# Optimization experiments

Hardware: AMD Instinct MI355X
Metric: run time of the kernel (lower is better)

Reference implementation:

```python
import jax, jax.numpy as jnp
import numpy as np

BN_EPS = 1e-5
NORM_EPS = 1e-12  # F.normalize eps
NUM_HEADS = 8
QUERY_DIM = 256
TOP_K = 16


def _l2norm(x):
    n = jnp.linalg.norm(x, axis=-1, keepdims=True)
    return x / jnp.maximum(n, NORM_EPS)


def setup_inputs() -> dict:
    key = jax.random.key(0)
    ks = jax.random.split(key, 8)
    B, S, D, O, N = 2, 512, 1024, 1024, 16384
    return {
        "hidden_states": jax.random.normal(ks[0], (B, S, D), jnp.float32),
        "Wq": jax.random.normal(ks[1], (D, NUM_HEADS * QUERY_DIM), jnp.float32) * 0.02,
        "bq": jnp.zeros((NUM_HEADS * QUERY_DIM,), jnp.float32),
        "bn_gamma": jnp.ones((QUERY_DIM,), jnp.float32),
        "bn_beta": jnp.zeros((QUERY_DIM,), jnp.float32),
        "sub_keys0": jax.random.normal(ks[2], (128, 128), jnp.float32) * 0.02,
        "sub_keys1": jax.random.normal(ks[3], (128, 128), jnp.float32) * 0.02,
        "expert_down": jax.random.normal(ks[4], (N, D), jnp.float32) * 0.02,
        "expert_up": jax.random.normal(ks[5], (N, O), jnp.float32) * 0.02,
    }


def reference(hidden_states, Wq, bq, bn_gamma, bn_beta, sub_keys0, sub_keys1, expert_down, expert_up):
    B, S, D = hidden_states.shape
    H, QD, K = NUM_HEADS, QUERY_DIM, TOP_K

    # query projection -> [B,S,H,QD]
    q = (hidden_states @ Wq + bq).reshape(B, S, H, QD)

    # BatchNorm1d over flattened (B*S*H, QD), training-mode batch stats (biased var)
    qf = q.reshape(-1, QD)
    mean = qf.mean(axis=0)
    var = qf.var(axis=0)
    qf = (qf - mean) * jax.lax.rsqrt(var + BN_EPS) * bn_gamma + bn_beta
    q = qf.reshape(B, S, H, QD)

    # split query into two halves, L2-normalize queries and keys, sub-scores
    half = QD // 2
    s0 = jnp.einsum('bshd,nd->bshn', _l2norm(q[..., :half]), _l2norm(sub_keys0))  # [B,S,H,128]
    s1 = jnp.einsum('bshd,nd->bshn', _l2norm(q[..., half:]), _l2norm(sub_keys1))  # [B,S,H,128]

    # cartesian-product scores: flat expert idx = i*128 + j (matches meshgrid 'ij')
    total = (s0[..., :, None] + s1[..., None, :]).reshape(B, S, H, -1)  # [B,S,H,16384]

    top_scores, top_idx = jax.lax.top_k(total, K)  # [B,S,H,K]
    w = jax.nn.softmax(top_scores, axis=-1)

    dw = expert_down[top_idx]  # [B,S,H,K,D]  (expert_hidden_size = 1)
    uw = expert_up[top_idx]    # [B,S,H,K,O]

    ei = jnp.einsum('bshkd,bsd->bshk', dw, hidden_states)  # per-expert scalar hidden
    eo = jax.nn.gelu(ei, approximate=False)                # F.gelu default = erf
    out = jnp.einsum('bshko,bshk,bshk->bso', uw, eo, w)    # weighted sum over K and H
    return out
```

## Files before the change

kernel.cpp:

```cpp
#include <hip/hip_runtime.h>
#include <math.h>

typedef unsigned long long u64;
typedef unsigned int u32;
typedef unsigned short ushort_t;
typedef _Float16 half8 __attribute__((ext_vector_type(8)));
typedef float f32x4 __attribute__((ext_vector_type(4)));

#define TOKENS 1024
#define DDIM   1024
#define NHEAD  8
#define QD     256
#define HQD    2048
#define NROWS  8192
#define NKEY   128
#define TOPK   16

#define QSCALE 256.0f
#define QINVS  (1.0f / 65536.0f)

__device__ __forceinline__ ushort_t f2bf(float f) {
    u32 u = __float_as_uint(f);
    u32 r = (u + 0x7FFFu + ((u >> 16) & 1u)) >> 16;
    return (ushort_t)r;
}
__device__ __forceinline__ float bf_lo(u32 w) { return __uint_as_float(w << 16); }
__device__ __forceinline__ float bf_hi(u32 w) { return __uint_as_float(w & 0xFFFF0000u); }

__device__ __forceinline__ void hsplit(float x, ushort_t& h, ushort_t& l) {
    _Float16 hh = (_Float16)x;
    float r = x - (float)hh;
    _Float16 ll = (_Float16)r;
    union { _Float16 f; ushort_t u; } c1, c2;
    c1.f = hh; c2.f = ll;
    h = c1.u; l = c2.u;
}

__device__ __forceinline__ u32 ordf(float v) {
    u32 u = __float_as_uint(v);
    return (u & 0x80000000u) ? ~u : (u | 0x80000000u);
}
__device__ __forceinline__ u64 mkkey2(float v, u32 idx) {
    return ((u64)ordf(v) << 32) | (u64)(0xFFFFFFFFu - idx);
}

template<int NTHR, int ITERS>
__device__ __forceinline__ void cvt_chunk(int gcb, int tid,
                                          const float* __restrict__ down,
                                          const float* __restrict__ up,
                                          ushort_t* __restrict__ downb,
                                          ushort_t* __restrict__ upb) {
    const float* src = (gcb < 1024) ? down : up;
    ushort_t* dst = (gcb < 1024) ? downb : upb;
    const size_t base4 = (size_t)(gcb & 1023) * 4096;
    const float4* s4 = (const float4*)src;
    ushort4* d4 = (ushort4*)dst;
#pragma unroll 4
    for (int it = 0; it < ITERS; it++) {
        size_t i = base4 + (size_t)it * NTHR + tid;
        float4 v = s4[i];
        ushort4 o;
        o.x = f2bf(v.x); o.y = f2bf(v.y); o.z = f2bf(v.z); o.w = f2bf(v.w);
        d4[i] = o;
    }
}

__global__ __launch_bounds__(256) void k_prep1(
    const float* __restrict__ A, const float* __restrict__ W,
    ushort_t* __restrict__ Ab, ushort_t* __restrict__ Wt,
    const float* __restrict__ sk0, const float* __restrict__ sk1,
    float* __restrict__ k0n, float* __restrict__ k1n)
{
    __shared__ __align__(16) char praw[18464];
    const int bid = blockIdx.x;
    const int tid = threadIdx.x;

    if (bid < 128) {
#pragma unroll
        for (int i = 0; i < 8; i++) {
            const int row = bid * 8 + i;
            float4 v = *(const float4*)(A + (size_t)row * 1024 + tid * 4);
            ushort4 h, l;
            hsplit(v.x * QSCALE, h.x, l.x);
            hsplit(v.y * QSCALE, h.y, l.y);
            hsplit(v.z * QSCALE, h.z, l.z);
            hsplit(v.w * QSCALE, h.w, l.w);
            *(ushort4*)(Ab + (size_t)row * 2048 + tid * 4) = h;
            *(ushort4*)(Ab + (size_t)row * 2048 + 1024 + tid * 4) = l;
        }
    } else if (bid < 640) {
        const int cb = bid - 128;
        const int k0 = (cb >> 5) * 64;
        const int n0 = (cb & 31) * 64;
        ushort_t* Lh = (ushort_t*)praw;
        ushort_t* Ll = (ushort_t*)praw + 4608;
        const int nn = (tid & 15) * 4;
        const int kk = tid >> 4;
#pragma unroll
        for (int p = 0; p < 4; p++) {
            const int k = kk + 16 * p;
            float4 v = *(const float4*)(W + (size_t)(k0 + k) * HQD + n0 + nn);
            float xs[4] = {v.x * QSCALE, v.y * QSCALE, v.z * QSCALE, v.w * QSCALE};
#pragma unroll
            for (int j = 0; j < 4; j++) {
                ushort_t h, l;
                hsplit(xs[j], h, l);
                Lh[(nn + j) * 72 + k] = h;
                Ll[(nn + j) * 72 + k] = l;
            }
        }
        __syncthreads();
#pragma unroll
        for (int e = 0; e < 2; e++) {
            const int idx = tid + 256 * e;
            const int n = idx >> 3, ks = idx & 7;
            uint4 hv = *(const uint4*)(Lh + n * 72 + ks * 8);
            uint4 lv = *(const uint4*)(Ll + n * 72 + ks * 8);
            *(uint4*)(Wt + (size_t)(n0 + n) * 2048 + k0 + ks * 8) = hv;
            *(uint4*)(Wt + (size_t)(n0 + n) * 2048 + 1024 + k0 + ks * 8) = lv;
        }
    } else {
        float* fs = (float*)praw;
        const int b2 = bid - 640;
        const int sub = tid >> 7;
        const int col = tid & 127;
        const int gr = b2 * 2 + sub;
        const float* src = (gr < 128) ? sk0 : sk1;
        float* dst = (gr < 128) ? k0n : k1n;
        const int row = gr & 127;
        float v = src[row * 128 + col];
        float sq = v * v;
        for (int off = 32; off; off >>= 1) sq += __shfl_down(sq, off);
        if ((tid & 63) == 0) fs[tid >> 6] = sq;
        __syncthreads();
        if ((tid & 127) == 0) {
            float n = sqrtf(fs[tid >> 6] + fs[(tid >> 6) + 1]);
            fs[8 + sub] = 1.0f / fmaxf(n, 1e-12f);
        }
        __syncthreads();
        dst[row * 128 + col] = v * fs[8 + sub];
    }
}

__global__ __launch_bounds__(256) void k_fused2(
    const ushort_t* __restrict__ Ab, const ushort_t* __restrict__ Wt,
    float* __restrict__ qp,
    const float* __restrict__ down, const float* __restrict__ up,
    ushort_t* __restrict__ downb, ushort_t* __restrict__ upb)
{
    __shared__ __align__(16) char lds[2][16384];
    const int tid = threadIdx.x;
    const int bid = blockIdx.x;

    if (bid >= 512) {
        cvt_chunk<256, 16>(bid - 512, tid, down, up, downb, upb);
        return;
    }

    const int m0 = (bid >> 5) * 64;
    const int n0 = (bid & 31) * 64;

    const int srow = tid >> 2;
    const int scol = (tid & 3) * 16;
    const int swz = (srow & 7) << 4;

    const int lane = tid & 63;
    const int w = tid >> 6;
    const int wmb = (w >> 1) * 32;
    const int wnb = (w & 1) * 32;
    const int fr = lane & 15;
    const int kg = lane >> 4;
    const int rswz = (fr & 7) << 4;

    f32x4 acc[2][2];
#pragma unroll
    for (int i = 0; i < 2; i++)
#pragma unroll
        for (int j = 0; j < 2; j++)
            acc[i][j] = (f32x4){0.f, 0.f, 0.f, 0.f};

    uint4 ar0, ar1, br0, br1;

    auto LOADR = [&](int gs) {
        const int term = gs >> 4;
        const int aoff = (term == 1) ? 1024 : 0;
        const int woff = (term == 2) ? 1024 : 0;
        const int kb = (gs & 15) * 64;
        const ushort_t* ap = Ab + (size_t)(m0 + srow) * 2048 + aoff + kb + scol;
        const ushort_t* wp = Wt + (size_t)(n0 + srow) * 2048 + woff + kb + scol;
        ar0 = *(const uint4*)(ap);
        ar1 = *(const uint4*)(ap + 8);
        br0 = *(const uint4*)(wp);
        br1 = *(const uint4*)(wp + 8);
    };
    auto WLDS = [&](int buf) {
        char* As = lds[buf];
        char* Bs = lds[buf] + 8192;
        const int b0 = (srow * 128 + scol * 2) ^ swz;
        const int b1 = (srow * 128 + scol * 2 + 16) ^ swz;
        *(uint4*)(As + b0) = ar0;
        *(uint4*)(As + b1) = ar1;
        *(uint4*)(Bs + b0) = br0;
        *(uint4*)(Bs + b1) = br1;
    };

    LOADR(0);
    WLDS(0);

    for (int s = 0; s < 48; s++) {
        __syncthreads();
        if (s < 47) LOADR(s + 1);
        const char* As = lds[s & 1];
        const char* Bs = lds[s & 1] + 8192;
#pragma unroll
        for (int kh = 0; kh < 2; kh++) {
            half8 a[2], b[2];
#pragma unroll
            for (int f = 0; f < 2; f++) {
                const int rowA = wmb + f * 16 + fr;
                a[f] = *(const half8*)(As + ((rowA * 128 + kh * 64 + kg * 16) ^ rswz));
                const int rowB = wnb + f * 16 + fr;
                b[f] = *(const half8*)(Bs + ((rowB * 128 + kh * 64 + kg * 16) ^ rswz));
            }
#pragma unroll
            for (int fm = 0; fm < 2; fm++)
#pragma unroll
                for (int fn = 0; fn < 2; fn++)
                    acc[fm][fn] = __builtin_amdgcn_mfma_f32_16x16x32_f16(
                        a[fm], b[fn], acc[fm][fn], 0, 0, 0);
        }
        if (s < 47) WLDS((s + 1) & 1);
    }

#pragma unroll
    for (int fm = 0; fm < 2; fm++) {
        const int rbase = m0 + wmb + fm * 16 + kg * 4;
#pragma unroll
        for (int fn = 0; fn < 2; fn++) {
            const int c = n0 + wnb + fn * 16 + fr;
#pragma unroll
            for (int j = 0; j < 4; j++)
                qp[(size_t)(rbase + j) * HQD + c] = acc[fm][fn][j];
        }
    }
}

__global__ __launch_bounds__(256) void k_bnstat1(const float* __restrict__ qp,
                                                 const float* __restrict__ bq,
                                                 float* __restrict__ psum,
                                                 float* __restrict__ psq,
                                                 float qsc,
                                                 const float* __restrict__ down,
                                                 const float* __restrict__ up,
                                                 ushort_t* __restrict__ downb,
                                                 ushort_t* __restrict__ upb)
{
    const int b = blockIdx.x;
    const int j = threadIdx.x;
    if (b >= 512) {
        cvt_chunk<256, 16>(512 + (b - 512), j, down, up, downb, upb);
        return;
    }
    float s = 0.f, sq = 0.f;
#pragma unroll 4
    for (int rr = 0; rr < 16; rr++) {
        const int r = b * 16 + rr;
        const size_t g = (size_t)r * 256 + j;
        float v = qp[g] * qsc + bq[(r & 7) * 256 + j];
        s += v; sq += v * v;
    }
    psum[b * 256 + j] = s;
    psq[b * 256 + j]  = sq;
}

__global__ __launch_bounds__(256) void k_bnstat2(const float* __restrict__ psum,
                                                 const float* __restrict__ psq,
                                                 const float* __restrict__ gamma,
                                                 float* __restrict__ meanOut,
                                                 float* __restrict__ scaleOut)
{
    __shared__ float ls[8][64];
    const int col = blockIdx.x * 32 + (threadIdx.x & 31);
    const int seg = threadIdx.x >> 5;
    float s = 0.f, sq = 0.f;
    for (int b = seg; b < 512; b += 8) {
        s += psum[b * 256 + col];
        sq += psq[b * 256 + col];
    }
    ls[seg][(threadIdx.x & 31)] = s;
    ls[seg][32 + (threadIdx.x & 31)] = sq;
    __syncthreads();
    if (threadIdx.x < 32) {
        float ts = 0.f, tq = 0.f;
#pragma unroll
        for (int g = 0; g < 8; g++) {
            ts += ls[g][threadIdx.x];
            tq += ls[g][32 + threadIdx.x];
        }
        float mean = ts * (1.0f / 8192.0f);
        float var = tq * (1.0f / 8192.0f) - mean * mean;
        meanOut[col] = mean;
        scaleOut[col] = gamma[col] / sqrtf(var + 1e-5f);
    }
}

__global__ __launch_bounds__(256) void k_scores(const float* __restrict__ qp,
                                                const float* __restrict__ bq,
                                                const float* __restrict__ mean,
                                                const float* __restrict__ scale,
                                                const float* __restrict__ beta,
                                                const float* __restrict__ kn0,
                                                const float* __restrict__ kn1,
                                                float* __restrict__ sOut0,
                                                float* __restrict__ sOut1,
                                                float qsc,
                                                const float* __restrict__ down,
                                                const float* __restrict__ up,
                                                ushort_t* __restrict__ downb,
                                                ushort_t* __restrict__ upb)
{
    __shared__ float Qs[128 * 68];
    __shared__ float Ks[64 * 132];
    __shared__ float rp[4][64];
    __shared__ float invn[64];
    const int bid = blockIdx.x;
    const int tid = threadIdx.x;
    if (bid >= 256) {
        cvt_chunk<256, 16>(768 + (bid - 256), tid, down, up, downb, upb);
        return;
    }
    const int half = bid >> 7;
    const int row0 = (bid & 127) * 64;

    {
        const int d4 = (tid & 31) * 4;
        const int rbase = tid >> 5;
        const int j4 = half * 128 + d4;
        float4 m4 = *(const float4*)(mean + j4);
        float4 sc4 = *(const float4*)(scale + j4);
        float4 be4 = *(const float4*)(beta + j4);
        float4 bi4 = *(const float4*)(bq + rbase * 256 + j4);
#pragma unroll
        for (int p = 0; p < 8; p++) {
            const int rr = rbase + p * 8;
            const int row = row0 + rr;
            const size_t g = (size_t)(row >> 3) * 2048 + (size_t)rbase * 256 + j4;
            float4 a = *(const float4*)(qp + g);
            float x0 = (a.x * qsc + bi4.x - m4.x) * sc4.x + be4.x;
            float x1 = (a.y * qsc + bi4.y - m4.y) * sc4.y + be4.y;
            float x2 = (a.z * qsc + bi4.z - m4.z) * sc4.z + be4.z;
            float x3 = (a.w * qsc + bi4.w - m4.w) * sc4.w + be4.w;
            Qs[(d4 + 0) * 68 + rr] = x0;
            Qs[(d4 + 1) * 68 + rr] = x1;
            Qs[(d4 + 2) * 68 + rr] = x2;
            Qs[(d4 + 3) * 68 + rr] = x3;
        }
    }
    __syncthreads();
    {
        const int r = tid & 63, qd = tid >> 6;
        float s = 0.f;
#pragma unroll 8
        for (int d = qd * 32; d < qd * 32 + 32; d++) {
            float v = Qs[d * 68 + r];
            s += v * v;
        }
        rp[qd][r] = s;
    }
    __syncthreads();
    if (tid < 64) {
        float s = rp[0][tid] + rp[1][tid] + rp[2][tid] + rp[3][tid];
        invn[tid] = 1.0f / fmaxf(sqrtf(s), 1e-12f);
    }

    const float* kn = half ? kn1 : kn0;
    float* sOut = half ? sOut1 : sOut0;
    const int ty = tid >> 5;
    const int tx = tid & 31;
    float acc[8][4] = {};

    for (int c = 0; c < 2; c++) {
        __syncthreads();
        {
            int dd4 = (tid & 15) * 4;
            int n = tid >> 4;
#pragma unroll
            for (int p = 0; p < 8; p++) {
                int nn = n + p * 16;
                float4 v = *(const float4*)(kn + nn * 128 + c * 64 + dd4);
                Ks[(dd4 + 0) * 132 + nn] = v.x; Ks[(dd4 + 1) * 132 + nn] = v.y;
                Ks[(dd4 + 2) * 132 + nn] = v.z; Ks[(dd4 + 3) * 132 + nn] = v.w;
            }
        }
        __syncthreads();
#pragma unroll
        for (int d = 0; d < 64; d++) {
            float a[8], b[4];
            *(float4*)(a)     = *(const float4*)&Qs[(c * 64 + d) * 68 + ty * 8];
            *(float4*)(a + 4) = *(const float4*)&Qs[(c * 64 + d) * 68 + ty * 8 + 4];
            *(float4*)(b)     = *(const float4*)&Ks[d * 132 + tx * 4];
#pragma unroll
            for (int i = 0; i < 8; i++)
#pragma unroll
                for (int j = 0; j < 4; j++)
                    acc[i][j] = fmaf(a[i], b[j], acc[i][j]);
        }
    }
#pragma unroll
    for (int i = 0; i < 8; i++) {
        const float iv = invn[ty * 8 + i];
        float4 r;
        r.x = acc[i][0] * iv; r.y = acc[i][1] * iv;
        r.z = acc[i][2] * iv; r.w = acc[i][3] * iv;
        *(float4*)(sOut + (size_t)(row0 + ty * 8 + i) * 128 + tx * 4) = r;
    }
}

__global__ __launch_bounds__(256) void k_topk(const float* __restrict__ s0,
                                              const float* __restrict__ s1,
                                              int* __restrict__ tIdx,
                                              float* __restrict__ tW,
                                              const float* __restrict__ down,
                                              const float* __restrict__ up,
                                              ushort_t* __restrict__ downb,
                                              ushort_t* __restrict__ upb)
{
    __shared__ float shv[4][2][16];
    __shared__ int   shi[4][2][16];
    __shared__ float swv[4][16];
    __shared__ u32   swi[4][16];
    const int bid = blockIdx.x;
    if (bid >= 2048) {
        cvt_chunk<256, 16>(1024 + (bid - 2048), threadIdx.x, down, up, downb, upb);
        return;
    }
    const int w = threadIdx.x >> 6;
    const int lane = threadIdx.x & 63;
    const int row = bid * 4 + w;
    const u64 below = (1ULL << lane) - 1;

    float v0[2], v1[2];
    u32 o0[2], o1[2], cur[2];
    v0[0] = s0[(size_t)row * 128 + lane];
    v1[0] = s0[(size_t)row * 128 + 64 + lane];
    v0[1] = s1[(size_t)row * 128 + lane];
    v1[1] = s1[(size_t)row * 128 + 64 + lane];
#pragma unroll
    for (int h = 0; h < 2; h++) {
        o0[h] = ordf(v0[h]); o1[h] = ordf(v1[h]); cur[h] = 0u;
    }
    for (int bit = 31; bit >= 0; --bit) {
#pragma unroll
        for (int h = 0; h < 2; h++) {
            u32 cand = cur[h] | (1u << bit);
            int c = __popcll(__ballot(o0[h] >= cand)) + __popcll(__ballot(o1[h] >= cand));
            if (c >= 16) cur[h] = cand;
        }
    }
#pragma unroll
    for (int h = 0; h < 2; h++) {
        u64 g0 = __ballot(o0[h] > cur[h]);
        u64 g1 = __ballot(o1[h] > cur[h]);
        const int cg0 = __popcll(g0);
        const int cntGT = cg0 + __popcll(g1);
        const int need = 16 - cntGT;
        u64 e0 = __ballot(o0[h] == cur[h]);
        u64 e1 = __ballot(o1[h] == cur[h]);
        const int ce0 = __popcll(e0);
        if (o0[h] > cur[h]) {
            int sl = __popcll(g0 & below);
            shv[w][h][sl] = v0[h]; shi[w][h][sl] = lane;
        }
        if (o1[h] > cur[h]) {
            int sl = cg0 + __popcll(g1 & below);
            shv[w][h][sl] = v1[h]; shi[w][h][sl] = lane + 64;
        }
        if (o0[h] == cur[h]) {
            int r = __popcll(e0 & below);
            if (r < need) { shv[w][h][cntGT + r] = v0[h]; shi[w][h][cntGT + r] = lane; }
        }
        if (o1[h] == cur[h]) {
            int r = ce0 + __popcll(e1 & below);
            if (r < need) { shv[w][h][cntGT + r] = v1[h]; shi[w][h][cntGT + r] = lane + 64; }
        }
    }

    float cv[4]; u32 ci[4], co[4];
#pragma unroll
    for (int qq = 0; qq < 4; qq++) {
        int id = lane + 64 * qq;
        int a = id >> 4, b = id & 15;
        cv[qq] = shv[w][0][a] + shv[w][1][b];
        ci[qq] = (u32)(shi[w][0][a] * 128 + shi[w][1][b]);
        co[qq] = ordf(cv[qq]);
    }
    u32 curV = 0;
    for (int bit = 31; bit >= 0; --bit) {
        u32 cand = curV | (1u << bit);
        int c = 0;
#pragma unroll
        for (int qq = 0; qq < 4; qq++) c += __popcll(__ballot(co[qq] >= cand));
        if (c >= 16) curV = cand;
    }
    bool gtf[4], eqf[4];
    int cntGT = 0;
#pragma unroll
    for (int qq = 0; qq < 4; qq++) {
        gtf[qq] = (co[qq] > curV);
        eqf[qq] = (co[qq] == curV);
        cntGT += __popcll(__ballot(gtf[qq]));
    }
    const int need = 16 - cntGT;
    u32 I = 0;
    for (int bit = 13; bit >= 0; --bit) {
        u32 cand = I | ((1u << bit) - 1u);
        int c = 0;
#pragma unroll
        for (int qq = 0; qq < 4; qq++)
            c += __popcll(__ballot(eqf[qq] && (ci[qq] <= cand)));
        if (c < need) I |= (1u << bit);
    }
    int pre = 0;
#pragma unroll
    for (int qq = 0; qq < 4; qq++) {
        bool sel = gtf[qq] || (eqf[qq] && (ci[qq] <= I));
        u64 sm = __ballot(sel);
        if (sel) {
            int sl = pre + __popcll(sm & below);
            swv[w][sl] = cv[qq]; swi[w][sl] = ci[qq];
        }
        pre += __popcll(sm);
    }

    if (lane < 16) {
        float myv = swv[w][lane];
        u32 myi = swi[w][lane];
        u64 myk = mkkey2(myv, myi);
        int rank = 0;
#pragma unroll
        for (int j = 0; j < 16; j++) {
            u64 kj = mkkey2(swv[w][j], swi[w][j]);
            rank += (kj > myk);
        }
        float vmax = myv;
#pragma unroll
        for (int off = 1; off < 16; off <<= 1)
            vmax = fmaxf(vmax, __shfl_xor(vmax, off, 16));
        float e = expf(myv - vmax);
        float ssum = e;
#pragma unroll
        for (int off = 1; off < 16; off <<= 1) ssum += __shfl_xor(ssum, off, 16);
        tW[(size_t)row * 16 + rank] = e / ssum;
        tIdx[(size_t)row * 16 + rank] = (int)myi;
    }
}

__global__ __launch_bounds__(1024) void k_coef_bf(const float* __restrict__ hidden,
                                                  const ushort_t* __restrict__ downb,
                                                  const int* __restrict__ tIdx,
                                                  const float* __restrict__ tW,
                                                  float* __restrict__ coef,
                                                  const float* __restrict__ down,
                                                  const float* __restrict__ up,
                                                  ushort_t* __restrict__ downb2,
                                                  ushort_t* __restrict__ upb)
{
    const int t = blockIdx.x;
    if (t >= 1024) {
        cvt_chunk<1024, 4>(1536 + (t - 1024), threadIdx.x, down, up, downb2, upb);
        return;
    }
    const int wave = threadIdx.x >> 6, lane = threadIdx.x & 63;
    const float* hp = hidden + (size_t)t * 1024;
    float h[16];
    *(float4*)(h + 0)  = *(const float4*)(hp + lane * 8);
    *(float4*)(h + 4)  = *(const float4*)(hp + lane * 8 + 4);
    *(float4*)(h + 8)  = *(const float4*)(hp + 512 + lane * 8);
    *(float4*)(h + 12) = *(const float4*)(hp + 512 + lane * 8 + 4);

#pragma unroll
    for (int g = 0; g < 2; g++) {
        const int pg = wave * 8 + g * 4;
        float s[4];
        uint4 a[4], b[4];
#pragma unroll
        for (int i = 0; i < 4; i++) {
            const int e = tIdx[(size_t)t * 128 + pg + i];
            const uint4* rp = (const uint4*)(downb + (size_t)e * 1024);
            a[i] = rp[lane];
            b[i] = rp[lane + 64];
        }
#pragma unroll
        for (int i = 0; i < 4; i++) {
            float acc = 0.f;
            const u32* aw = (const u32*)&a[i];
            const u32* bw = (const u32*)&b[i];
#pragma unroll
            for (int c = 0; c < 4; c++) {
                acc = fmaf(bf_lo(aw[c]), h[2 * c], acc);
                acc = fmaf(bf_hi(aw[c]), h[2 * c + 1], acc);
                acc = fmaf(bf_lo(bw[c]), h[8 + 2 * c], acc);
                acc = fmaf(bf_hi(bw[c]), h[8 + 2 * c + 1], acc);
            }
            s[i] = acc;
        }
#pragma unroll
        for (int i = 0; i < 4; i++)
#pragma unroll
            for (int off = 1; off < 64; off <<= 1) s[i] += __shfl_xor(s[i], off);
        if (lane < 4) {
            float x = (lane == 0) ? s[0] : (lane == 1) ? s[1] : (lane == 2) ? s[2] : s[3];
            float wv = tW[(size_t)t * 128 + pg + lane];
            float gl = 0.5f * x * (1.0f + erff(x * 0.70710678118654752f));
            coef[(size_t)t * 128 + pg + lane] = wv * gl;
        }
    }
}

__global__ __launch_bounds__(1024) void k_coef_f32(const float* __restrict__ hidden,
                                                   const float* __restrict__ down,
                                                   const int* __restrict__ tIdx,
                                                   const float* __restrict__ tW,
                                                   float* __restrict__ coef)
{
    __shared__ __align__(16) float hs[1024];
    __shared__ int   eidx[128];
    __shared__ float wv[128];
    const int t = blockIdx.x;
    const int tid = threadIdx.x;
    hs[tid] = hidden[(size_t)t * 1024 + tid];
    if (tid < 128) {
        eidx[tid] = tIdx[(size_t)t * 128 + tid];
        wv[tid]   = tW[(size_t)t * 128 + tid];
    }
    __syncthreads();
    const int wave = tid >> 6, lane = tid & 63;
#pragma unroll 2
    for (int i = 0; i < 8; i++) {
        const int p = wave * 8 + i;
        const float4* dp = (const float4*)(down + (size_t)eidx[p] * 1024);
        float sum = 0.f;
#pragma unroll
        for (int c = 0; c < 4; c++) {
            float4 dv = dp[lane + 64 * c];
            float4 hv = *(const float4*)(hs + (lane + 64 * c) * 4);
            sum += dv.x * hv.x + dv.y * hv.y + dv.z * hv.z + dv.w * hv.w;
        }
        for (int off = 32; off; off >>= 1) sum += __shfl_down(sum, off);
        if (lane == 0) {
            float x = sum;
            float g = 0.5f * x * (1.0f + erff(x * 0.70710678118654752f));
            coef[(size_t)t * 128 + p] = wv[p] * g;
        }
    }
}

__global__ __launch_bounds__(256) void k_accum_bf(const ushort_t* __restrict__ upb,
                                                  const int* __restrict__ tIdx,
                                                  const float* __restrict__ coef,
                                                  float* __restrict__ out)
{
    __shared__ float cf[128];
    __shared__ int   ei[128];
    __shared__ float part[512];
    const int t = blockIdx.x >> 1;
    const int jh = blockIdx.x & 1;
    const int tid = threadIdx.x;
    if (tid < 128) {
        cf[tid] = coef[(size_t)t * 128 + tid];
        ei[tid] = tIdx[(size_t)t * 128 + tid];
    }
    __syncthreads();
    const int half = tid >> 7;
    const int jl = (tid & 127) * 4;
    const int j4 = jh * 512 + jl;
    float acc[4] = {};
    const int p0 = half * 64;
#pragma unroll 16
    for (int p = p0; p < p0 + 64; p++) {
        const float c = cf[p];
        uint2 v = *(const uint2*)(upb + (size_t)ei[p] * 1024 + j4);
        acc[0] = fmaf(c, bf_lo(v.x), acc[0]);
        acc[1] = fmaf(c, bf_hi(v.x), acc[1]);
        acc[2] = fmaf(c, bf_lo(v.y), acc[2]);
        acc[3] = fmaf(c, bf_hi(v.y), acc[3]);
    }
    if (half == 0) *(float4*)&part[jl] = *(float4*)acc;
    __syncthreads();
    if (half == 1) {
        float4 pv = *(float4*)&part[jl];
        float4 r;
        r.x = acc[0] + pv.x; r.y = acc[1] + pv.y;
        r.z = acc[2] + pv.z; r.w = acc[3] + pv.w;
        *(float4*)(out + (size_t)t * 1024 + j4) = r;
    }
}

__global__ __launch_bounds__(256) void k_accum_f32(const float* __restrict__ up,
                                                   const int* __restrict__ tIdx,
                                                   const float* __restrict__ coef,
                                                   float* __restrict__ out)
{
    __shared__ float cf[128];
    __shared__ int   ei[128];
    const int t = blockIdx.x >> 2;
    const int c = blockIdx.x & 3;
    const int tid = threadIdx.x;
    if (tid < 128) {
        cf[tid] = coef[(size_t)t * 128 + tid];
        ei[tid] = tIdx[(size_t)t * 128 + tid];
    }
    __syncthreads();
    const int j = c * 256 + tid;
    float acc = 0.f;
#pragma unroll 8
    for (int p = 0; p < 128; p++)
        acc = fmaf(cf[p], up[(size_t)ei[p] * 1024 + j], acc);
    out[(size_t)t * 1024 + j] = acc;
}

__global__ __launch_bounds__(256) void k_fall1(
    const float* __restrict__ A, const float* __restrict__ W,
    float* __restrict__ qp,
    const float* __restrict__ sk0, const float* __restrict__ sk1,
    float* __restrict__ k0n, float* __restrict__ k1n)
{
    __shared__ float smem[2 * 32 * 68];
    const int bid = blockIdx.x;
    const int tid = threadIdx.x;

    if (bid < 512) {
        float* As = smem;
        float* Bs = smem + 32 * 68;
        const int m0 = (bid >> 5) * 64;
        const int n0 = (bid & 31) * 64;
        const int aM  = tid >> 3;
        const int aK4 = (tid & 7) * 4;
        const int bK  = tid >> 4;
        const int bN4 = (tid & 15) * 4;
        const int ty  = tid >> 4;
        const int tx  = tid & 15;
        float acc[4][4] = {};
        for (int kk = 0; kk < 1024; kk += 32) {
            __syncthreads();
#pragma unroll
            for (int p = 0; p < 2; p++) {
                int m = aM + 32 * p;
                float4 v = *(const float4*)(A + (size_t)(m0 + m) * DDIM + kk + aK4);
                As[(aK4 + 0) * 68 + m] = v.x; As[(aK4 + 1) * 68 + m] = v.y;
                As[(aK4 + 2) * 68 + m] = v.z; As[(aK4 + 3) * 68 + m] = v.w;
            }
#pragma unroll
            for (int p = 0; p < 2; p++) {
                int k = bK + 16 * p;
                float4 v = *(const float4*)(W + (size_t)(kk + k) * HQD + n0 + bN4);
                *(float4*)&Bs[k * 68 + bN4] = v;
            }
            __syncthreads();
#pragma unroll
            for (int k = 0; k < 32; k++) {
                float a[4], b[4];
                *(float4*)(a) = *(const float4*)&As[k * 68 + ty * 4];
                *(float4*)(b) = *(const float4*)&Bs[k * 68 + tx * 4];
#pragma unroll
                for (int i = 0; i < 4; i++)
#pragma unroll
                    for (int j = 0; j < 4; j++)
                        acc[i][j] = fmaf(a[i], b[j], acc[i][j]);
            }
        }
#pragma unroll
        for (int i = 0; i < 4; i++) {
            int m = m0 + ty * 4 + i;
            float4 r;
            r.x = acc[i][0]; r.y = acc[i][1]; r.z = acc[i][2]; r.w = acc[i][3];
            *(float4*)(qp + (size_t)m * HQD + n0 + tx * 4) = r;
        }
    } else {
        const int b2 = bid - 512;
        const int sub = tid >> 7;
        const int col = tid & 127;
        const int gr = b2 * 2 + sub;
        const float* src = (gr < 128) ? sk0 : sk1;
        float* dst = (gr < 128) ? k0n : k1n;
        const int row = gr & 127;
        float v = src[row * 128 + col];
        float sq = v * v;
        for (int off = 32; off; off >>= 1) sq += __shfl_down(sq, off);
        if ((tid & 63) == 0) smem[tid >> 6] = sq;
        __syncthreads();
        if ((tid & 127) == 0) {
            float n = sqrtf(smem[tid >> 6] + smem[(tid >> 6) + 1]);
            smem[8 + sub] = 1.0f / fmaxf(n, 1e-12f);
        }
        __syncthreads();
        dst[row * 128 + col] = v * smem[8 + sub];
    }
}

extern "C" void kernel_launch(void* const* d_in, const int* in_sizes, int n_in,
                              void* d_out, int out_size, void* d_ws, size_t ws_size,
                              hipStream_t stream)
{
    const float* hidden = (const float*)d_in[0];
    const float* Wq     = (const float*)d_in[1];
    const float* bq     = (const float*)d_in[2];
    const float* gamma  = (const float*)d_in[3];
    const float* beta   = (const float*)d_in[4];
    const float* sk0    = (const float*)d_in[5];
    const float* sk1    = (const float*)d_in[6];
    const float* down   = (const float*)d_in[7];
    const float* up     = (const float*)d_in[8];
    float* out = (float*)d_out;

    float* ws = (float*)d_ws;
    size_t o = 0;
    float* qp    = ws + o; o += (size_t)TOKENS * HQD;
    float* ps    = ws + o; o += 512 * 256;
    float* pq    = ws + o; o += 512 * 256;
    float* meanb = ws + o; o += 256;
    float* scaleb= ws + o; o += 256;
    float* k0n   = ws + o; o += NKEY * 128;
    float* k1n   = ws + o; o += NKEY * 128;
    float* s0    = ws + o; o += (size_t)NROWS * 128;
    float* s1    = ws + o; o += (size_t)NROWS * 128;
    float* tW    = ws + o; o += (size_t)NROWS * TOPK;
    int*   tIdx  = (int*)(ws + o); o += (size_t)NROWS * TOPK;
    float* coef  = ws + o; o += (size_t)TOKENS * 128;
    ushort_t* downb = (ushort_t*)(ws + o); o += (size_t)16384 * 1024 / 2;
    ushort_t* upb   = (ushort_t*)(ws + o); o += (size_t)16384 * 1024 / 2;
    ushort_t* Ab    = (ushort_t*)(ws + o); o += (size_t)1024 * 2048 / 2;
    ushort_t* Wt    = (ushort_t*)(ws + o); o += (size_t)2048 * 2048 / 2;
    const int useBF = (ws_size >= o * sizeof(float)) ? 1 : 0;
    const float qsc = useBF ? QINVS : 1.0f;

    if (useBF) {
        k_prep1 <<<768, 256, 0, stream>>>(hidden, Wq, Ab, Wt, sk0, sk1, k0n, k1n);
        k_fused2<<<1024, 256, 0, stream>>>(Ab, Wt, qp, down, up, downb, upb);
        k_bnstat1<<<768, 256, 0, stream>>>(qp, bq, ps, pq, qsc, down, up, downb, upb);
        k_bnstat2<<<8, 256, 0, stream>>>(ps, pq, gamma, meanb, scaleb);
        k_scores <<<512, 256, 0, stream>>>(qp, bq, meanb, scaleb, beta,
                                           k0n, k1n, s0, s1, qsc,
                                           down, up, downb, upb);
        k_topk   <<<2560, 256, 0, stream>>>(s0, s1, tIdx, tW, down, up, downb, upb);
        k_coef_bf<<<1536, 1024, 0, stream>>>(hidden, downb, tIdx, tW, coef,
                                             down, up, downb, upb);
        k_accum_bf<<<2048, 256, 0, stream>>>(upb, tIdx, coef, out);
    } else {
        k_fall1 <<<640, 256, 0, stream>>>(hidden, Wq, qp, sk0, sk1, k0n, k1n);
        k_bnstat1<<<512, 256, 0, stream>>>(qp, bq, ps, pq, qsc, down, up, downb, upb);
        k_bnstat2<<<8, 256, 0, stream>>>(ps, pq, gamma, meanb, scaleb);
        k_scores <<<256, 256, 0, stream>>>(qp, bq, meanb, scaleb, beta,
                                           k0n, k1n, s0, s1, qsc,
                                           down, up, downb, upb);
        k_topk   <<<2048, 256, 0, stream>>>(s0, s1, tIdx, tW, down, up, downb, upb);
        k_coef_f32 <<<TOKENS, 1024, 0, stream>>>(hidden, down, tIdx, tW, coef);
        k_accum_f32<<<4096, 256, 0, stream>>>(up, tIdx, coef, out);
    }
}
```

Baseline: 183.3 us.

## Fuse expert coefficient and up-projection accumulation into one per-token kernel

Measured after the change: 186.8 us. About the same (+1.9%).

```diff
diff --git a/kernel.cpp b/kernel.cpp
--- a/kernel.cpp
+++ b/kernel.cpp
@@ -431,7 +431,7 @@
     __shared__ u32   swi[4][16];
     const int bid = blockIdx.x;
     if (bid >= 2048) {
-        cvt_chunk<256, 16>(1024 + (bid - 2048), threadIdx.x, down, up, downb, upb);
+        cvt_chunk<256, 16>(1536 + (bid - 2048), threadIdx.x, down, up, downb, upb);
         return;
     }
     const int w = threadIdx.x >> 6;
@@ -555,22 +555,22 @@
     }
 }
 
-__global__ __launch_bounds__(1024) void k_coef_bf(const float* __restrict__ hidden,
-                                                  const ushort_t* __restrict__ downb,
-                                                  const int* __restrict__ tIdx,
-                                                  const float* __restrict__ tW,
-                                                  float* __restrict__ coef,
-                                                  const float* __restrict__ down,
-                                                  const float* __restrict__ up,
-                                                  ushort_t* __restrict__ downb2,
-                                                  ushort_t* __restrict__ upb)
-{
+__global__ __launch_bounds__(1024) void k_mlp_bf(const float* __restrict__ hidden,
+                                                 const ushort_t* __restrict__ downb,
+                                                 const ushort_t* __restrict__ upb,
+                                                 const int* __restrict__ tIdx,
+                                                 const float* __restrict__ tW,
+                                                 float* __restrict__ out)
+{
+    __shared__ float cf[128];
+    __shared__ int   ei[128];
+    __shared__ float part[3 * 1024];
     const int t = blockIdx.x;
-    if (t >= 1024) {
-        cvt_chunk<1024, 4>(1536 + (t - 1024), threadIdx.x, down, up, downb2, upb);
-        return;
-    }
-    const int wave = threadIdx.x >> 6, lane = threadIdx.x & 63;
+    const int tid = threadIdx.x;
+    const int wave = tid >> 6, lane = tid & 63;
+
+    if (tid < 128) ei[tid] = tIdx[(size_t)t * 128 + tid];
+
     const float* hp = hidden + (size_t)t * 1024;
     float h[16];
     *(float4*)(h + 0)  = *(const float4*)(hp + lane * 8);
@@ -612,8 +612,36 @@
             float x = (lane == 0) ? s[0] : (lane == 1) ? s[1] : (lane == 2) ? s[2] : s[3];
             float wv = tW[(size_t)t * 128 + pg + lane];
             float gl = 0.5f * x * (1.0f + erff(x * 0.70710678118654752f));
-            coef[(size_t)t * 128 + pg + lane] = wv * gl;
-        }
+            cf[pg + lane] = wv * gl;
+        }
+    }
+    __syncthreads();
+
+    const int q = tid >> 8;
+    const int jl = (tid & 255) * 4;
+    float acc[4] = {};
+    const int p0 = q * 32;
+#pragma unroll 8
+    for (int p = p0; p < p0 + 32; p++) {
+        const float c = cf[p];
+        uint2 v = *(const uint2*)(upb + (size_t)ei[p] * 1024 + jl);
+        acc[0] = fmaf(c, bf_lo(v.x), acc[0]);
+        acc[1] = fmaf(c, bf_hi(v.x), acc[1]);
+        acc[2] = fmaf(c, bf_lo(v.y), acc[2]);
+        acc[3] = fmaf(c, bf_hi(v.y), acc[3]);
+    }
+    if (q) *(float4*)&part[(q - 1) * 1024 + jl] = *(float4*)acc;
+    __syncthreads();
+    if (q == 0) {
+        float4 p0v = *(float4*)&part[jl];
+        float4 p1v = *(float4*)&part[1024 + jl];
+        float4 p2v = *(float4*)&part[2048 + jl];
+        float4 r;
+        r.x = acc[0] + p0v.x + p1v.x + p2v.x;
+        r.y = acc[1] + p0v.y + p1v.y + p2v.y;
+        r.z = acc[2] + p0v.z + p1v.z + p2v.z;
+        r.w = acc[3] + p0v.w + p1v.w + p2v.w;
+        *(float4*)(out + (size_t)t * 1024 + jl) = r;
     }
 }
 
@@ -652,47 +680,6 @@
             float g = 0.5f * x * (1.0f + erff(x * 0.70710678118654752f));
             coef[(size_t)t * 128 + p] = wv[p] * g;
         }
-    }
-}
-
-__global__ __launch_bounds__(256) void k_accum_bf(const ushort_t* __restrict__ upb,
-                                                  const int* __restrict__ tIdx,
-                                                  const float* __restrict__ coef,
-                                                  float* __restrict__ out)
-{
-    __shared__ float cf[128];
-    __shared__ int   ei[128];
-    __shared__ float part[512];
-    const int t = blockIdx.x >> 1;
-    const int jh = blockIdx.x & 1;
-    const int tid = threadIdx.x;
-    if (tid < 128) {
-        cf[tid] = coef[(size_t)t * 128 + tid];
-        ei[tid] = tIdx[(size_t)t * 128 + tid];
-    }
-    __syncthreads();
-    const int half = tid >> 7;
-    const int jl = (tid & 127) * 4;
-    const int j4 = jh * 512 + jl;
-    float acc[4] = {};
-    const int p0 = half * 64;
-#pragma unroll 16
-    for (int p = p0; p < p0 + 64; p++) {
-        const float c = cf[p];
-        uint2 v = *(const uint2*)(upb + (size_t)ei[p] * 1024 + j4);
-        acc[0] = fmaf(c, bf_lo(v.x), acc[0]);
-        acc[1] = fmaf(c, bf_hi(v.x), acc[1]);
-        acc[2] = fmaf(c, bf_lo(v.y), acc[2]);
-        acc[3] = fmaf(c, bf_hi(v.y), acc[3]);
-    }
-    if (half == 0) *(float4*)&part[jl] = *(float4*)acc;
-    __syncthreads();
-    if (half == 1) {
-        float4 pv = *(float4*)&part[jl];
-        float4 r;
-        r.x = acc[0] + pv.x; r.y = acc[1] + pv.y;
-        r.z = acc[2] + pv.z; r.w = acc[3] + pv.w;
-        *(float4*)(out + (size_t)t * 1024 + j4) = r;
     }
 }
 
@@ -839,13 +826,11 @@
         k_fused2<<<1024, 256, 0, stream>>>(Ab, Wt, qp, down, up, downb, upb);
         k_bnstat1<<<768, 256, 0, stream>>>(qp, bq, ps, pq, qsc, down, up, downb, upb);
         k_bnstat2<<<8, 256, 0, stream>>>(ps, pq, gamma, meanb, scaleb);
-        k_scores <<<512, 256, 0, stream>>>(qp, bq, meanb, scaleb, beta,
-                                           k0n, k1n, s0, s1, qsc,
-                                           down, up, downb, upb);
+        k_scores <<<1024, 256, 0, stream>>>(qp, bq, meanb, scaleb, beta,
+                                            k0n, k1n, s0, s1, qsc,
+                                            down, up, downb, upb);
         k_topk   <<<2560, 256, 0, stream>>>(s0, s1, tIdx, tW, down, up, downb, upb);
-        k_coef_bf<<<1536, 1024, 0, stream>>>(hidden, downb, tIdx, tW, coef,
-                                             down, up, downb, upb);
-        k_accum_bf<<<2048, 256, 0, stream>>>(upb, tIdx, coef, out);
+        k_mlp_bf <<<TOKENS, 1024, 0, stream>>>(hidden, downb, upb, tIdx, tW, out);
     } else {
         k_fall1 <<<640, 256, 0, stream>>>(hidden, Wq, qp, sk0, sk1, k0n, k1n);
         k_bnstat1<<<512, 256, 0, stream>>>(qp, bq, ps, pq, qsc, down, up, downb, upb);
```
